# Optimization experiments

Measured on AMD Instinct MI355X. Metric: run time of the kernel, lower is better.

## Reference

```python
import jax, jax.numpy as jnp
import numpy as np

SIGMA_SPATIAL = 1.0
SIGMA_BILATERAL = 0.25
RADIUS = 1
PATCH = 2 * RADIUS + 1  # 3


def _spatial_kernel():
    x, y = np.mgrid[-RADIUS:RADIUS + 1, -RADIUS:RADIUS + 1]
    w1 = np.exp(-(x ** 2 + y ** 2) / (2.0 * SIGMA_SPATIAL ** 2))
    return jnp.asarray(w1.reshape(-1), dtype=jnp.float32)  # [PATCH*PATCH]


def _extract_patches(x):
    # x: [B,H,W,C] -> [B,H,W,PATCH*PATCH,C] via reflect-padded shifted slices
    B, H, W, C = x.shape
    xp = jnp.pad(x, ((0, 0), (RADIUS, RADIUS), (RADIUS, RADIUS), (0, 0)), mode='reflect')
    return jnp.stack(
        [xp[:, dy:dy + H, dx:dx + W, :] for dy in range(PATCH) for dx in range(PATCH)],
        axis=3,
    )


def setup_inputs() -> dict:
    key = jax.random.key(0)
    k1, k2 = jax.random.split(key)
    src = jax.random.uniform(k1, (2, 512, 512, 21), dtype=jnp.float32)
    im = jax.random.uniform(k2, (2, 512, 512, 3), dtype=jnp.float32)
    return {"src": src, "im": im}


def reference(src, im):
    w1 = _spatial_kernel()  # [9]
    im_patches = _extract_patches(im)                      # [B,H,W,9,Ci]
    diff2 = jnp.sum((im_patches - im[:, :, :, None, :]) ** 2, axis=-1)  # [B,H,W,9]
    w = jnp.exp(-diff2 / (2.0 * SIGMA_BILATERAL ** 2)) * w1            # [B,H,W,9]
    src_patches = _extract_patches(src)                    # [B,H,W,9,Cs]
    num = jnp.sum(src_patches * w[..., None], axis=3)      # [B,H,W,Cs]
    den = jnp.sum(w, axis=3, keepdims=True)                # [B,H,W,1]
    return num / den
```

## Files before the change

### kernel.cpp

```cpp
#include <hip/hip_runtime.h>

#define BATCH 2
#define H 512
#define W 512
#define CS 21
#define CI 3
#define P 256
#define TPB 256
#define NCH 6

__device__ __forceinline__ void fma4(float4& a, const float4 v, const float w) {
    a.x = fmaf(v.x, w, a.x);
    a.y = fmaf(v.y, w, a.y);
    a.z = fmaf(v.z, w, a.z);
    a.w = fmaf(v.w, w, a.w);
}

__global__ __launch_bounds__(TPB, 8) void jbu_kernel(
    const float* __restrict__ src, const float* __restrict__ im,
    float* __restrict__ out)
{
    __shared__ __align__(16) float s_buf[P * 12];

    const int t = threadIdx.x;

    const int f   = blockIdx.x;
    const int xcd = f & 7;
    const int g   = f >> 3;
    const int y   = (xcd << 6) | (g & 63);
    const int r   = g >> 6;
    const int x0  = (r & 1) * P;
    const int b   = r >> 1;

    const int ry0 = (y == 0)     ? 1     : y - 1;
    const int ry2 = (y == H - 1) ? H - 2 : y + 1;

    const float* imb = im + (size_t)b * H * W * CI;
    for (int i = t; i < 3 * (P + 2) * CI; i += TPB) {
        int row = i / ((P + 2) * CI);
        int rem = i - row * ((P + 2) * CI);
        int col = rem / CI;
        int ch  = rem - col * CI;
        int ry  = (row == 0) ? ry0 : ((row == 1) ? y : ry2);
        int gx  = x0 + col - 1;
        gx = (gx < 0) ? 1 : ((gx >= W) ? W - 2 : gx);
        s_buf[i] = imb[(ry * W + gx) * CI + ch];
    }
    __syncthreads();

    float4 wa, wb;
    float w8n;
    {
        const float w1k[9] = {0.36787944f, 0.60653066f, 0.36787944f,
                              0.60653066f, 1.0f,        0.60653066f,
                              0.36787944f, 0.60653066f, 0.36787944f};
        const int cbase = ((P + 2) + t + 1) * CI;
        const float c0 = s_buf[cbase + 0];
        const float c1 = s_buf[cbase + 1];
        const float c2 = s_buf[cbase + 2];
        float wv[9];
        float den = 0.f;
        #pragma unroll
        for (int k = 0; k < 9; ++k) {
            const int dy = k / 3, dx = k % 3;
            const int idx = (dy * (P + 2) + t + dx) * CI;
            float d0 = s_buf[idx + 0] - c0;
            float d1 = s_buf[idx + 1] - c1;
            float d2 = s_buf[idx + 2] - c2;
            float w = __expf(-8.0f * (d0 * d0 + d1 * d1 + d2 * d2)) * w1k[k];
            wv[k] = w;
            den += w;
        }
        const float inv = 1.0f / den;
        wa = make_float4(wv[0] * inv, wv[1] * inv, wv[2] * inv, wv[3] * inv);
        wb = make_float4(wv[4] * inv, wv[5] * inv, wv[6] * inv, wv[7] * inv);
        w8n = wv[8] * inv;
    }
    __syncthreads();

    *(float4*)&s_buf[t * 12 + 0] = wa;
    *(float4*)&s_buf[t * 12 + 4] = wb;
    s_buf[t * 12 + 8] = w8n;
    __syncthreads();

    const float* row0 = src + (size_t)(b * H + ry0) * (W * CS);
    const float* row1 = src + (size_t)(b * H + y  ) * (W * CS);
    const float* row2 = src + (size_t)(b * H + ry2) * (W * CS);
    float*       orow = out + (size_t)(b * H + y  ) * (W * CS);

    for (int wi = t; wi < P * NCH; wi += TPB) {
        int p = wi / NCH;
        int q = wi - p * NCH;
        int coff = (q == 5) ? 17 : (q << 2);
        int x  = x0 + p;
        int xm = (x == 0)     ? 1     : x - 1;
        int xp = (x == W - 1) ? W - 2 : x + 1;
        int om = xm * CS + coff;
        int oc = x  * CS + coff;
        int op = xp * CS + coff;

        const float4 pwA = *(const float4*)&s_buf[p * 12 + 0];
        const float4 pwB = *(const float4*)&s_buf[p * 12 + 4];
        const float  pw8 = s_buf[p * 12 + 8];

        float4 v0 = *(const float4*)(row0 + om);
        float4 v1 = *(const float4*)(row0 + oc);
        float4 v2 = *(const float4*)(row0 + op);
        float4 v3 = *(const float4*)(row1 + om);
        float4 v4 = *(const float4*)(row1 + oc);
        float4 v5 = *(const float4*)(row1 + op);
        float4 v6 = *(const float4*)(row2 + om);
        float4 v7 = *(const float4*)(row2 + oc);
        float4 v8 = *(const float4*)(row2 + op);

        float4 acc = {0.f, 0.f, 0.f, 0.f};
        fma4(acc, v0, pwA.x);
        fma4(acc, v1, pwA.y);
        fma4(acc, v2, pwA.z);
        fma4(acc, v3, pwA.w);
        fma4(acc, v4, pwB.x);
        fma4(acc, v5, pwB.y);
        fma4(acc, v6, pwB.z);
        fma4(acc, v7, pwB.w);
        fma4(acc, v8, pw8);

        *(float4*)(orow + oc) = acc;
    }
}

extern "C" void kernel_launch(void* const* d_in, const int* in_sizes, int n_in,
                              void* d_out, int out_size, void* d_ws, size_t ws_size,
                              hipStream_t stream) {
    const float* src = (const float*)d_in[0];
    const float* im  = (const float*)d_in[1];
    float* out = (float*)d_out;
    dim3 grid((W / P) * H * BATCH, 1, 1);
    jbu_kernel<<<grid, TPB, 0, stream>>>(src, im, out);
}
```

Before: 112.6 us.

## Stage 3x130 src tile in shared memory and halve columns per block

After: 151.4 us. 34.5% more time.

```diff
diff --git a/kernel.cpp b/kernel.cpp
--- a/kernel.cpp
+++ b/kernel.cpp
@@ -5,9 +5,11 @@
 #define W 512
 #define CS 21
 #define CI 3
-#define P 256
+#define P 128
 #define TPB 256
-#define NCH 6
+#define SLOTS (P + 2)
+#define STRIDE 28
+#define GSZ (3 * SLOTS * CI)
 
 __device__ __forceinline__ void fma4(float4& a, const float4 v, const float w) {
     a.x = fmaf(v.x, w, a.x);
@@ -16,11 +18,12 @@
     a.w = fmaf(v.w, w, a.w);
 }
 
-__global__ __launch_bounds__(TPB, 8) void jbu_kernel(
+__global__ __launch_bounds__(TPB, 3) void jbu_kernel(
     const float* __restrict__ src, const float* __restrict__ im,
     float* __restrict__ out)
 {
-    __shared__ __align__(16) float s_buf[P * 12];
+    __shared__ __align__(16) float s_src[3 * SLOTS * STRIDE];
+    __shared__ __align__(16) float s_w[P * 12];
 
     const int t = threadIdx.x;
 
@@ -28,103 +31,120 @@
     const int xcd = f & 7;
     const int g   = f >> 3;
     const int y   = (xcd << 6) | (g & 63);
-    const int r   = g >> 6;
-    const int x0  = (r & 1) * P;
-    const int b   = r >> 1;
+    const int rem = g >> 6;
+    const int x0  = (rem & 3) << 7;
+    const int b   = rem >> 2;
 
     const int ry0 = (y == 0)     ? 1     : y - 1;
     const int ry2 = (y == H - 1) ? H - 2 : y + 1;
 
-    const float* imb = im + (size_t)b * H * W * CI;
-    for (int i = t; i < 3 * (P + 2) * CI; i += TPB) {
-        int row = i / ((P + 2) * CI);
-        int rem = i - row * ((P + 2) * CI);
-        int col = rem / CI;
-        int ch  = rem - col * CI;
-        int ry  = (row == 0) ? ry0 : ((row == 1) ? y : ry2);
-        int gx  = x0 + col - 1;
-        gx = (gx < 0) ? 1 : ((gx >= W) ? W - 2 : gx);
-        s_buf[i] = imb[(ry * W + gx) * CI + ch];
+    {
+        const float* imb = im + (size_t)b * (H * W * CI);
+        for (int i = t; i < GSZ; i += TPB) {
+            int r    = i / (SLOTS * CI);
+            int remi = i - r * (SLOTS * CI);
+            int slot = remi / CI;
+            int ch   = remi - slot * CI;
+            int ry   = (r == 0) ? ry0 : ((r == 1) ? y : ry2);
+            int gx   = x0 + slot - 1;
+            gx = (gx < 0) ? 1 : ((gx >= W) ? W - 2 : gx);
+            s_w[i] = imb[(ry * W + gx) * CI + ch];
+        }
+    }
+
+    {
+        for (int i = t; i < 3 * SLOTS * 6; i += TPB) {
+            int r    = i / (SLOTS * 6);
+            int remi = i - r * (SLOTS * 6);
+            int slot = remi / 6;
+            int q    = remi - slot * 6;
+            int ry   = (r == 0) ? ry0 : ((r == 1) ? y : ry2);
+            int gx   = x0 + slot - 1;
+            gx = (gx < 0) ? 1 : ((gx >= W) ? W - 2 : gx);
+            const float* srow = src + ((size_t)(b * H + ry) * W + gx) * CS;
+            float* dst = &s_src[(r * SLOTS + slot) * STRIDE];
+            if (q < 5) {
+                *(float4*)(dst + (q << 2)) = *(const float4*)(srow + (q << 2));
+            } else {
+                dst[20] = srow[20];
+            }
+        }
     }
     __syncthreads();
 
     float4 wa, wb;
-    float w8n;
-    {
+    float  w8n;
+    if (t < P) {
         const float w1k[9] = {0.36787944f, 0.60653066f, 0.36787944f,
                               0.60653066f, 1.0f,        0.60653066f,
                               0.36787944f, 0.60653066f, 0.36787944f};
-        const int cbase = ((P + 2) + t + 1) * CI;
-        const float c0 = s_buf[cbase + 0];
-        const float c1 = s_buf[cbase + 1];
-        const float c2 = s_buf[cbase + 2];
+        const int cbase = (SLOTS + t + 1) * CI;
+        const float c0 = s_w[cbase + 0];
+        const float c1 = s_w[cbase + 1];
+        const float c2 = s_w[cbase + 2];
         float wv[9];
         float den = 0.f;
         #pragma unroll
         for (int k = 0; k < 9; ++k) {
             const int dy = k / 3, dx = k % 3;
-            const int idx = (dy * (P + 2) + t + dx) * CI;
-            float d0 = s_buf[idx + 0] - c0;
-            float d1 = s_buf[idx + 1] - c1;
-            float d2 = s_buf[idx + 2] - c2;
+            const int idx = (dy * SLOTS + t + dx) * CI;
+            float d0 = s_w[idx + 0] - c0;
+            float d1 = s_w[idx + 1] - c1;
+            float d2 = s_w[idx + 2] - c2;
             float w = __expf(-8.0f * (d0 * d0 + d1 * d1 + d2 * d2)) * w1k[k];
             wv[k] = w;
             den += w;
         }
         const float inv = 1.0f / den;
-        wa = make_float4(wv[0] * inv, wv[1] * inv, wv[2] * inv, wv[3] * inv);
-        wb = make_float4(wv[4] * inv, wv[5] * inv, wv[6] * inv, wv[7] * inv);
+        wa  = make_float4(wv[0] * inv, wv[1] * inv, wv[2] * inv, wv[3] * inv);
+        wb  = make_float4(wv[4] * inv, wv[5] * inv, wv[6] * inv, wv[7] * inv);
         w8n = wv[8] * inv;
+    } else {
+        for (int i = t - P; i < 3 * SLOTS; i += TPB - P) {
+            float* pd = &s_src[i * STRIDE + 21];
+            pd[0] = 0.f; pd[1] = 0.f; pd[2] = 0.f;
+        }
     }
     __syncthreads();
 
-    *(float4*)&s_buf[t * 12 + 0] = wa;
-    *(float4*)&s_buf[t * 12 + 4] = wb;
-    s_buf[t * 12 + 8] = w8n;
+    if (t < P) {
+        *(float4*)&s_w[t * 12 + 0] = wa;
+        *(float4*)&s_w[t * 12 + 4] = wb;
+        s_w[t * 12 + 8] = w8n;
+    }
     __syncthreads();
 
-    const float* row0 = src + (size_t)(b * H + ry0) * (W * CS);
-    const float* row1 = src + (size_t)(b * H + y  ) * (W * CS);
-    const float* row2 = src + (size_t)(b * H + ry2) * (W * CS);
-    float*       orow = out + (size_t)(b * H + y  ) * (W * CS);
+    float* orow = out + (size_t)(b * H + y) * (W * CS) + x0 * CS;
 
-    for (int wi = t; wi < P * NCH; wi += TPB) {
-        int p = wi / NCH;
-        int q = wi - p * NCH;
-        int coff = (q == 5) ? 17 : (q << 2);
-        int x  = x0 + p;
-        int xm = (x == 0)     ? 1     : x - 1;
-        int xp = (x == W - 1) ? W - 2 : x + 1;
-        int om = xm * CS + coff;
-        int oc = x  * CS + coff;
-        int op = xp * CS + coff;
+    #pragma unroll
+    for (int it = 0; it < 3; ++it) {
+        int item = it * TPB + t;
+        int p = item / 6;
+        int q = item - p * 6;
+        int qoff = q << 2;
 
-        const float4 pwA = *(const float4*)&s_buf[p * 12 + 0];
-        const float4 pwB = *(const float4*)&s_buf[p * 12 + 4];
-        const float  pw8 = s_buf[p * 12 + 8];
+        const float4 pwA = *(const float4*)&s_w[p * 12 + 0];
+        const float4 pwB = *(const float4*)&s_w[p * 12 + 4];
+        const float  pw8 = s_w[p * 12 + 8];
 
-        float4 v0 = *(const float4*)(row0 + om);
-        float4 v1 = *(const float4*)(row0 + oc);
-        float4 v2 = *(const float4*)(row0 + op);
-        float4 v3 = *(const float4*)(row1 + om);
-        float4 v4 = *(const float4*)(row1 + oc);
-        float4 v5 = *(const float4*)(row1 + op);
-        float4 v6 = *(const float4*)(row2 + om);
-        float4 v7 = *(const float4*)(row2 + oc);
-        float4 v8 = *(const float4*)(row2 + op);
+        const float* base0 = &s_src[(0 * SLOTS + p) * STRIDE + qoff];
+        const float* base1 = &s_src[(1 * SLOTS + p) * STRIDE + qoff];
+        const float* base2 = &s_src[(2 * SLOTS + p) * STRIDE + qoff];
 
         float4 acc = {0.f, 0.f, 0.f, 0.f};
-        fma4(acc, v0, pwA.x);
-        fma4(acc, v1, pwA.y);
-        fma4(acc, v2, pwA.z);
-        fma4(acc, v3, pwA.w);
-        fma4(acc, v4, pwB.x);
-        fma4(acc, v5, pwB.y);
-        fma4(acc, v6, pwB.z);
-        fma4(acc, v7, pwB.w);
-        fma4(acc, v8, pw8);
+        fma4(acc, *(const float4*)(base0             ), pwA.x);
+        fma4(acc, *(const float4*)(base0 +     STRIDE), pwA.y);
+        fma4(acc, *(const float4*)(base0 + 2 * STRIDE), pwA.z);
+        fma4(acc, *(const float4*)(base1             ), pwA.w);
+        fma4(acc, *(const float4*)(base1 +     STRIDE), pwB.x);
+        fma4(acc, *(const float4*)(base1 + 2 * STRIDE), pwB.y);
+        fma4(acc, *(const float4*)(base2             ), pwB.z);
+        fma4(acc, *(const float4*)(base2 +     STRIDE), pwB.w);
+        fma4(acc, *(const float4*)(base2 + 2 * STRIDE), pw8);
 
-        *(float4*)(orow + oc) = acc;
+        float* op = orow + p * CS + qoff;
+        if (q < 5) *(float4*)op = acc;
+        else       *op = acc.x;
     }
 }
 
```
